# Kernel optimization log

Measured on AMD Instinct MI355X. Metric: run time of the kernel, lower is better.

Reference implementation:

```python
import jax, jax.numpy as jnp
import numpy as np
from jax import lax

HID = 256
CB_N = 512   # codebook_size
CB_D = 64    # codebook_dim
FC = 6       # force_channels
COMMIT_W = 0.25


def _conv(x, w, b, stride):
    # x: [B,C,H,W], w: [O,I,3,3], 'same'-style padding=1
    y = lax.conv_general_dilated(x, w, (stride, stride), ((1, 1), (1, 1)),
                                 dimension_numbers=('NCHW', 'OIHW', 'NCHW'))
    return y + b[None, :, None, None]


def _silu(x):
    return x * jax.nn.sigmoid(x)


def setup_inputs() -> dict:
    key = jax.random.key(0)
    ks = jax.random.split(key, 8)
    s = 0.05
    force_field = jax.random.normal(ks[0], (8, FC, 256, 256), dtype=jnp.float32)
    w1 = jax.random.normal(ks[1], (HID, FC, 3, 3), dtype=jnp.float32) * s
    b1 = jnp.zeros((HID,), dtype=jnp.float32)
    w2 = jax.random.normal(ks[2], (HID, HID, 3, 3), dtype=jnp.float32) * s
    b2 = jnp.zeros((HID,), dtype=jnp.float32)
    w3 = jax.random.normal(ks[3], (CB_D, HID, 3, 3), dtype=jnp.float32) * s
    b3 = jnp.zeros((CB_D,), dtype=jnp.float32)
    codebook = jax.random.uniform(ks[4], (CB_N, CB_D), dtype=jnp.float32,
                                  minval=-1.0 / CB_N, maxval=1.0 / CB_N)
    return {"force_field": force_field, "w1": w1, "b1": b1, "w2": w2,
            "b2": b2, "w3": w3, "b3": b3, "codebook": codebook}


def reference(force_field, w1, b1, w2, b2, w3, b3, codebook):
    # Encoder: conv(pad1) -> SiLU -> conv(stride2) -> SiLU -> conv(stride2)
    h = _silu(_conv(force_field, w1, b1, 1))
    h = _silu(_conv(h, w2, b2, 2))
    z = _conv(h, w3, b3, 2)                      # [B, CB_D, h, w]
    B, C, hh, ww = z.shape
    z_flat = jnp.transpose(z, (0, 2, 3, 1)).reshape(-1, C)  # [N, CB_D]
    # pairwise squared distances: ||z||^2 + ||c||^2 - 2 z.c
    dists = (jnp.sum(z_flat * z_flat, axis=1, keepdims=True)
             + jnp.sum(codebook * codebook, axis=1)
             - 2.0 * (z_flat @ codebook.T))      # [N, CB_N]
    indices = jnp.argmin(dists, axis=1)          # [N] int
    z_q = codebook[indices].reshape(B, hh, ww, C).transpose(0, 3, 1, 2)
    commitment_loss = (jnp.mean((lax.stop_gradient(z_q) - z) ** 2)
                       + COMMIT_W * jnp.mean((z_q - lax.stop_gradient(z)) ** 2))
    tokens = indices.reshape(B, hh, ww)
    return tokens, commitment_loss
```

## Files before the change

### kernel.cpp

```cpp
#include <hip/hip_runtime.h>
#include <math.h>


#define FC    6
#define HID   256
#define CB_N  512
#define CB_D  64

typedef _Float16 f16x8 __attribute__((ext_vector_type(8)));
typedef _Float16 f16x4 __attribute__((ext_vector_type(4)));
typedef float f32x16 __attribute__((ext_vector_type(16)));

#define H1N_IMG    17105920
#define H2N_IMG    4359168

#define FFP_ROW    260
#define FFP_CI     (258 * FFP_ROW)
#define FFP_IMG    (6 * FFP_CI)

__global__ void fill_sentinel_kernel(float* out, int n) {
    int i = blockIdx.x * 256 + threadIdx.x;
    if (i < n) out[i] = -12345.0f;
}

__global__ void h1n_guard_kernel(unsigned int* h1n, int nslots) {
    int i = blockIdx.x * 256 + threadIdx.x;
    if (i >= nslots * 132096) return;
    int slot = i / 132096;
    int r    = i - slot * 132096;
    unsigned int* base = h1n + (size_t)slot * H1N_IMG;
    if (r < 66560) base[r] = 0u;
    else {
        int r2  = r - 66560;
        int j   = r2 & 3;
        int hl  = (r2 >> 2) & 1;
        int cg  = (r2 >> 3) & 31;
        int row = (r2 >> 8) + 1;
        base[(size_t)row * 66560 + 33280 + cg * 1040 + hl * 520 + j] = 0u;
    }
}

__global__ void h2n_guard_kernel(unsigned int* h2n, int nslots) {
    int i = blockIdx.x * 256 + threadIdx.x;
    if (i >= nslots * 66560) return;
    int slot = i / 66560;
    int r    = i - slot * 66560;
    unsigned int* base = h2n + (size_t)slot * H2N_IMG;
    if (r < 33792) base[r] = 0u;
    else {
        int r2  = r - 33792;
        int j   = r2 & 3;
        int hl  = (r2 >> 2) & 1;
        int cg  = (r2 >> 3) & 31;
        int row = (r2 >> 8) + 1;
        base[(size_t)row * 33792 + 16896 + cg * 528 + hl * 264 + j] = 0u;
    }
}

__global__ void wswz1_kernel(const float* __restrict__ w1, _Float16* __restrict__ wsz) {
    int i = blockIdx.x * 256 + threadIdx.x;
    if (i >= 2 * 4 * 4096) return;
    int j   = i & 7;
    int co_ = (i >> 3) & 127;
    int kc  = (i >> 10) & 1;
    int hf  = (i >> 11) & 1;
    int st  = (i >> 12) & 3;
    int ct  = i >> 14;
    int k   = st * 16 + kc * 8 + j;
    int co  = ct * 128 + co_;
    float v = (k < 54) ? w1[(size_t)co * 54 + k] : 0.f;
    _Float16 h = (_Float16)v;
    _Float16 l = (_Float16)(v - (float)h);
    wsz[i] = hf ? l : h;
}

__global__ void wswz2_kernel(const float* __restrict__ w2, _Float16* __restrict__ wsz) {
    int i = blockIdx.x * 256 + threadIdx.x;
    if (i >= 2 * 144 * 4096) return;
    int j   = i & 7;
    int co_ = (i >> 3) & 127;
    int kc  = (i >> 10) & 1;
    int hf  = (i >> 11) & 1;
    int st  = (i >> 12) % 144;
    int ct  = (i >> 12) / 144;
    int ci  = (st & 15) * 16 + kc * 8 + j;
    int rs  = st >> 4;
    float v = w2[(size_t)(ct * 128 + co_) * 2304 + ci * 9 + rs];
    _Float16 h = (_Float16)v;
    _Float16 l = (_Float16)(v - (float)h);
    wsz[i] = hf ? l : h;
}

__global__ void wswz3_kernel(const float* __restrict__ w3, _Float16* __restrict__ wsz) {
    int i = blockIdx.x * 256 + threadIdx.x;
    if (i >= 144 * 2048) return;
    int j  = i & 7;
    int co = (i >> 3) & 63;
    int kc = (i >> 9) & 1;
    int hf = (i >> 10) & 1;
    int st = i >> 11;
    int ci = (st & 15) * 16 + kc * 8 + j;
    int rs = st >> 4;
    float v = w3[(size_t)co * 2304 + ci * 9 + rs];
    _Float16 h = (_Float16)v;
    _Float16 l = (_Float16)(v - (float)h);
    wsz[i] = hf ? l : h;
}

__global__ void cnorm_kernel(const float* __restrict__ cb, float* __restrict__ cn) {
    int j = blockIdx.x * 256 + threadIdx.x;
    if (j < CB_N) {
        const float* p = cb + j * CB_D;
        float s0 = 0.f, s1 = 0.f, s2 = 0.f, s3 = 0.f;
        for (int i = 0; i < CB_D; i += 4) {
            s0 = fmaf(p[i],   p[i],   s0);
            s1 = fmaf(p[i+1], p[i+1], s1);
            s2 = fmaf(p[i+2], p[i+2], s2);
            s3 = fmaf(p[i+3], p[i+3], s3);
        }
        cn[j] = (s0 + s1) + (s2 + s3);
    }
}

__device__ __forceinline__ float silu_f(float v) {
    return v / (1.f + expf(-v));
}

__device__ __forceinline__ unsigned int pack_hl(float v) {
    _Float16 h = (_Float16)v;
    _Float16 l = (_Float16)(v - (float)h);
    unsigned short hb = __builtin_bit_cast(unsigned short, h);
    unsigned short lb = __builtin_bit_cast(unsigned short, l);
    return (unsigned int)hb | ((unsigned int)lb << 16);
}

__device__ __forceinline__ f16x8 as_f16x8(uint4 v) {
    return __builtin_bit_cast(f16x8, v);
}

__device__ __forceinline__ unsigned int ldu32_sb(const char* base, unsigned off, int px) {
    return *(const unsigned int*)(base + (unsigned)__builtin_amdgcn_readfirstlane((int)off) + px * 4);
}

__device__ __forceinline__ void sync_lds() {
    asm volatile("s_waitcnt lgkmcnt(0)\n\ts_barrier" ::: "memory");
}

__global__ __launch_bounds__(256) void ffpack_kernel(const float* __restrict__ ff,
                                                     unsigned int* __restrict__ ffp) {
    const int gw   = (blockIdx.x * 256 + threadIdx.x) >> 6;
    const int lane = threadIdx.x & 63;
    const int y  = gw & 255;
    const int ic = gw >> 8;
    const float* rowp = ff + ((size_t)ic * 256 + y) * 256;
    float4 v = *(const float4*)(rowp + 4 * lane);
    unsigned p0 = pack_hl(v.x), p1 = pack_hl(v.y), p2 = pack_hl(v.z), p3 = pack_hl(v.w);
    unsigned p3p = __shfl_up(p3, 1);
    if (lane == 0) p3p = 0u;
    unsigned int* orow = ffp + ((size_t)ic * 258 + y + 1) * FFP_ROW;
    uint4 o; o.x = p3p; o.y = p0; o.z = p1; o.w = p2;
    *(uint4*)(orow + 4 * lane) = o;
    if (lane == 63) { orow[256] = p3; orow[257] = 0u; }
}

__global__ __launch_bounds__(256) void conv1_mfma_kernel(
        const unsigned int* __restrict__ ffp,
        const _Float16* __restrict__ wsz1,
        const float* __restrict__ bias,
        unsigned int* __restrict__ h1n,
        int b0) {
    __shared__ __align__(16) _Float16 ldsA[2][2][128][8];
    __shared__ __align__(16) _Float16 ldsB[2][128][24];
    __shared__ __align__(16) unsigned int T[64];
    __shared__ float biasl[128];

    const int tid = threadIdx.x;
    const int py  = blockIdx.x >> 1;
    const int xt  = blockIdx.x & 1;
    const int ct  = blockIdx.y;
    const int img = blockIdx.z;

    const unsigned int* ffpi = ffp + (size_t)(b0 + img) * FFP_IMG;
    _Float16* h1f = (_Float16*)(h1n + (size_t)img * H1N_IMG);

    if (tid < 64) {
        int k = tid;
        unsigned off;
        if (k < 54) {
            int ci  = k / 9;
            int tap = k - ci * 9;
            int r   = tap / 3;
            int s   = tap - r * 3;
            off = (unsigned)((((size_t)ci * 258 + py + r) * FFP_ROW + xt * 128 + s) * 4);
        } else {
            off = (unsigned)((xt * 128) * 4);
        }
        T[k] = off;
    }
    if (tid < 128) biasl[tid] = bias[ct * 128 + tid];
    __syncthreads();

    const int lane = tid & 63;
    const int w    = tid >> 6;
    const int cow  = (w >> 1) * 64;
    const int pxw  = (w & 1) * 64;
    const int m_   = lane & 31;
    const int kc   = lane >> 5;
    const int px   = tid & 127;
    const int kh   = tid >> 7;

    f32x16 acc[2][2];
    #pragma unroll
    for (int a = 0; a < 2; a++)
        #pragma unroll
        for (int b = 0; b < 2; b++)
            #pragma unroll
            for (int r = 0; r < 16; r++) acc[a][b][r] = 0.f;

    uint4* aldsf = (uint4*)&ldsA[0][0][0][0];
    const char* gbase = (const char*)ffpi;

    uint4 a0, a1;
    unsigned v0, v1, v2, v3, v4, v5, v6, v7;
    {
        const uint4* ag = (const uint4*)(wsz1 + ((size_t)(ct * 4)) * 4096);
        a0 = ag[tid];
        a1 = ag[tid + 256];
        const int k0 = kh * 8;
        uint4 rb0 = *(const uint4*)&T[k0];
        uint4 rb1 = *(const uint4*)&T[k0 + 4];
        v0 = ldu32_sb(gbase, rb0.x, px); v1 = ldu32_sb(gbase, rb0.y, px);
        v2 = ldu32_sb(gbase, rb0.z, px); v3 = ldu32_sb(gbase, rb0.w, px);
        v4 = ldu32_sb(gbase, rb1.x, px); v5 = ldu32_sb(gbase, rb1.y, px);
        v6 = ldu32_sb(gbase, rb1.z, px); v7 = ldu32_sb(gbase, rb1.w, px);
    }

    for (int t = 0; t < 4; t++) {
        sync_lds();

        aldsf[tid]       = a0;
        aldsf[tid + 256] = a1;
        uint4 bh, bl;
        bh.x = (v0 & 0xffffu) | (v1 << 16);
        bh.y = (v2 & 0xffffu) | (v3 << 16);
        bh.z = (v4 & 0xffffu) | (v5 << 16);
        bh.w = (v6 & 0xffffu) | (v7 << 16);
        bl.x = (v0 >> 16) | (v1 & 0xffff0000u);
        bl.y = (v2 >> 16) | (v3 & 0xffff0000u);
        bl.z = (v4 >> 16) | (v5 & 0xffff0000u);
        bl.w = (v6 >> 16) | (v7 & 0xffff0000u);
        *(uint4*)&ldsB[0][px][kh * 8] = bh;
        *(uint4*)&ldsB[1][px][kh * 8] = bl;

        sync_lds();

        if (t < 3) {
            const uint4* ag = (const uint4*)(wsz1 + ((size_t)(ct * 4 + t + 1)) * 4096);
            a0 = ag[tid];
            a1 = ag[tid + 256];
            const int k0 = (t + 1) * 16 + kh * 8;
            uint4 rb0 = *(const uint4*)&T[k0 & 63];
            uint4 rb1 = *(const uint4*)&T[(k0 + 4) & 63];
            v0 = ldu32_sb(gbase, rb0.x, px); v1 = ldu32_sb(gbase, rb0.y, px);
            v2 = ldu32_sb(gbase, rb0.z, px); v3 = ldu32_sb(gbase, rb0.w, px);
            v4 = ldu32_sb(gbase, rb1.x, px); v5 = ldu32_sb(gbase, rb1.y, px);
            v6 = ldu32_sb(gbase, rb1.z, px); v7 = ldu32_sb(gbase, rb1.w, px);
        }

        f16x8 ah0 = *(const f16x8*)&ldsA[0][kc][cow + m_][0];
        f16x8 ah1 = *(const f16x8*)&ldsA[0][kc][cow + 32 + m_][0];
        f16x8 al0 = *(const f16x8*)&ldsA[1][kc][cow + m_][0];
        f16x8 al1 = *(const f16x8*)&ldsA[1][kc][cow + 32 + m_][0];
        f16x8 xh0 = *(const f16x8*)&ldsB[0][pxw + m_][kc * 8];
        f16x8 xh1 = *(const f16x8*)&ldsB[0][pxw + 32 + m_][kc * 8];
        f16x8 xl0 = *(const f16x8*)&ldsB[1][pxw + m_][kc * 8];
        f16x8 xl1 = *(const f16x8*)&ldsB[1][pxw + 32 + m_][kc * 8];

        acc[0][0] = __builtin_amdgcn_mfma_f32_32x32x16_f16(ah0, xh0, acc[0][0], 0, 0, 0);
        acc[0][1] = __builtin_amdgcn_mfma_f32_32x32x16_f16(ah0, xh1, acc[0][1], 0, 0, 0);
        acc[1][0] = __builtin_amdgcn_mfma_f32_32x32x16_f16(ah1, xh0, acc[1][0], 0, 0, 0);
        acc[1][1] = __builtin_amdgcn_mfma_f32_32x32x16_f16(ah1, xh1, acc[1][1], 0, 0, 0);
        acc[0][0] = __builtin_amdgcn_mfma_f32_32x32x16_f16(ah0, xl0, acc[0][0], 0, 0, 0);
        acc[0][1] = __builtin_amdgcn_mfma_f32_32x32x16_f16(ah0, xl1, acc[0][1], 0, 0, 0);
        acc[1][0] = __builtin_amdgcn_mfma_f32_32x32x16_f16(ah1, xl0, acc[1][0], 0, 0, 0);
        acc[1][1] = __builtin_amdgcn_mfma_f32_32x32x16_f16(ah1, xl1, acc[1][1], 0, 0, 0);
        acc[0][0] = __builtin_amdgcn_mfma_f32_32x32x16_f16(al0, xh0, acc[0][0], 0, 0, 0);
        acc[0][1] = __builtin_amdgcn_mfma_f32_32x32x16_f16(al0, xh1, acc[0][1], 0, 0, 0);
        acc[1][0] = __builtin_amdgcn_mfma_f32_32x32x16_f16(al1, xh0, acc[1][0], 0, 0, 0);
        acc[1][1] = __builtin_amdgcn_mfma_f32_32x32x16_f16(al1, xh1, acc[1][1], 0, 0, 0);
    }

    #pragma unroll
    for (int mt = 0; mt < 2; mt++) {
        #pragma unroll
        for (int nt = 0; nt < 2; nt++) {
            const int pxo = xt * 128 + pxw + nt * 32 + m_;
            const int par = pxo & 1;
            const int xs  = par ? ((pxo + 1) >> 1) : (pxo >> 1);
            _Float16* dst = h1f + (size_t)(py + 1) * 133120 + par * 66560 + xs * 8 + kc * 4;
            #pragma unroll
            for (int q = 0; q < 4; q++) {
                const int cb_ = cow + mt * 32 + 8 * q + 4 * kc;
                const int cg  = (ct * 128 + cow + mt * 32 + 8 * q) >> 3;
                f16x4 oh, ol;
                #pragma unroll
                for (int j = 0; j < 4; j++) {
                    float v = silu_f(acc[mt][nt][4*q+j] + biasl[cb_ + j]);
                    _Float16 h = (_Float16)v;
                    oh[j] = h;
                    ol[j] = (_Float16)(v - (float)h);
                }
                *(f16x4*)(dst + (size_t)cg * 2080)        = oh;
                *(f16x4*)(dst + (size_t)cg * 2080 + 1040) = ol;
            }
        }
    }
}

__global__ __launch_bounds__(256) void conv2_mfma_kernel(
        const unsigned int* __restrict__ h1n,
        const _Float16* __restrict__ wsz2,
        const float* __restrict__ bias,
        unsigned int* __restrict__ h2n) {
    __shared__ __align__(16) char ldsB[2 * 16384];
    __shared__ float biasl[128];

    const int tid = threadIdx.x;
    const int py  = blockIdx.x;
    const int ct  = blockIdx.y;
    const int img = blockIdx.z;

    if (tid < 128) biasl[tid] = bias[ct * 128 + tid];

    const int lane = tid & 63;
    const int w    = tid >> 6;
    const int cow  = (w >> 1) * 64;
    const int pxw  = (w & 1) * 64;
    const int m_   = lane & 31;
    const int kc   = lane >> 5;

    const char* bbase = (const char*)(h1n + (size_t)img * H1N_IMG);
    const char* abase = (const char*)wsz2 + (size_t)ct * 144 * 8192
                        + (size_t)kc * 2048 + (size_t)(cow + m_) * 16;

    const int spx = tid & 127;
    const int skc = tid >> 7;
    const unsigned sgfix = (unsigned)(skc * 4160 + spx * 16);
    const unsigned swfix = (unsigned)(skc * 2048 + spx * 16);
    const unsigned rfix0 = (unsigned)(kc * 2048 + (pxw + m_) * 16);
    const unsigned rfix1 = (unsigned)(kc * 2048 + (pxw + 32 + m_) * 16);

    auto offu = [&](int t) -> unsigned {
        int rs = t >> 4;
        int r  = (rs * 11) >> 5;
        int s  = rs - 3 * r;
        return (unsigned)((2 * py + r) * 266240 + (s != 1 ? 133120 : 0)
                          + (s == 2 ? 16 : 0) + (t & 15) * 8320);
    };

    f32x16 acc[2][2];
    #pragma unroll
    for (int a = 0; a < 2; a++)
        #pragma unroll
        for (int b = 0; b < 2; b++)
            #pragma unroll
            for (int r = 0; r < 16; r++) acc[a][b][r] = 0.f;

    uint4 pa0, pa1, pa2, pa3;
    uint4 wa0, wa1, wa2, wa3;
    uint4 wb0, wb1, wb2, wb3;
    {
        pa0 = *(const uint4*)(abase);
        pa1 = *(const uint4*)(abase + 512);
        pa2 = *(const uint4*)(abase + 4096);
        pa3 = *(const uint4*)(abase + 4096 + 512);
        unsigned o0 = offu(0);
        uint4 th = *(const uint4*)(bbase + o0 + sgfix);
        uint4 tl = *(const uint4*)(bbase + o0 + sgfix + 2080);
        *(uint4*)(ldsB + swfix)        = th;
        *(uint4*)(ldsB + 4096 + swfix) = tl;
        unsigned o1 = offu(1);
        th = *(const uint4*)(bbase + o1 + sgfix);
        tl = *(const uint4*)(bbase + o1 + sgfix + 2080);
        *(uint4*)(ldsB + 8192 + swfix)  = th;
        *(uint4*)(ldsB + 12288 + swfix) = tl;
        unsigned o2 = offu(2);
        wa0 = *(const uint4*)(bbase + o2 + sgfix);
        wa1 = *(const uint4*)(bbase + o2 + sgfix + 2080);
        unsigned o3 = offu(3);
        wa2 = *(const uint4*)(bbase + o3 + sgfix);
        wa3 = *(const uint4*)(bbase + o3 + sgfix + 2080);
        unsigned o4 = offu(4);
        wb0 = *(const uint4*)(bbase + o4 + sgfix);
        wb1 = *(const uint4*)(bbase + o4 + sgfix + 2080);
        unsigned o5 = offu(5);
        wb2 = *(const uint4*)(bbase + o5 + sgfix);
        wb3 = *(const uint4*)(bbase + o5 + sgfix + 2080);
    }
    sync_lds();

    auto superstep = [&](int s, uint4& W0, uint4& W1, uint4& W2, uint4& W3) {
        const int t0 = 2 * s;
        char* rslot = ldsB + (s & 1) * 16384;

        if (s < 71) {
            char* wslot = ldsB + ((s + 1) & 1) * 16384;
            *(uint4*)(wslot + swfix)         = W0;
            *(uint4*)(wslot + 4096 + swfix)  = W1;
            *(uint4*)(wslot + 8192 + swfix)  = W2;
            *(uint4*)(wslot + 12288 + swfix) = W3;
        }
        if (s < 69) {
            unsigned oa = offu(t0 + 6);
            unsigned ob = offu(t0 + 7);
            W0 = *(const uint4*)(bbase + oa + sgfix);
            W1 = *(const uint4*)(bbase + oa + sgfix + 2080);
            W2 = *(const uint4*)(bbase + ob + sgfix);
            W3 = *(const uint4*)(bbase + ob + sgfix + 2080);
        }

        f16x8 xh0 = *(const f16x8*)(rslot + rfix0);
        f16x8 xl0 = *(const f16x8*)(rslot + 4096 + rfix0);
        f16x8 xh1 = *(const f16x8*)(rslot + rfix1);
        f16x8 xl1 = *(const f16x8*)(rslot + 4096 + rfix1);

        uint4 ca0 = pa0, ca1 = pa1, ca2 = pa2, ca3 = pa3;
        {
            const char* ap = abase + (size_t)(t0 + 1) * 8192;
            pa0 = *(const uint4*)(ap);
            pa1 = *(const uint4*)(ap + 512);
            pa2 = *(const uint4*)(ap + 4096);
            pa3 = *(const uint4*)(ap + 4096 + 512);
        }

        f16x8 ah0 = as_f16x8(ca0);
        f16x8 ah1 = as_f16x8(ca1);
        f16x8 al0 = as_f16x8(ca2);
        f16x8 al1 = as_f16x8(ca3);

        acc[0][0] = __builtin_amdgcn_mfma_f32_32x32x16_f16(ah0, xh0, acc[0][0], 0, 0, 0);
        acc[0][1] = __builtin_amdgcn_mfma_f32_32x32x16_f16(ah0, xh1, acc[0][1], 0, 0, 0);
        acc[1][0] = __builtin_amdgcn_mfma_f32_32x32x16_f16(ah1, xh0, acc[1][0], 0, 0, 0);
        acc[1][1] = __builtin_amdgcn_mfma_f32_32x32x16_f16(ah1, xh1, acc[1][1], 0, 0, 0);
        acc[0][0] = __builtin_amdgcn_mfma_f32_32x32x16_f16(ah0, xl0, acc[0][0], 0, 0, 0);
        acc[0][1] = __builtin_amdgcn_mfma_f32_32x32x16_f16(ah0, xl1, acc[0][1], 0, 0, 0);
        acc[1][0] = __builtin_amdgcn_mfma_f32_32x32x16_f16(ah1, xl0, acc[1][0], 0, 0, 0);
        acc[1][1] = __builtin_amdgcn_mfma_f32_32x32x16_f16(ah1, xl1, acc[1][1], 0, 0, 0);
        acc[0][0] = __builtin_amdgcn_mfma_f32_32x32x16_f16(al0, xh0, acc[0][0], 0, 0, 0);
        acc[0][1] = __builtin_amdgcn_mfma_f32_32x32x16_f16(al0, xh1, acc[0][1], 0, 0, 0);
        acc[1][0] = __builtin_amdgcn_mfma_f32_32x32x16_f16(al1, xh0, acc[1][0], 0, 0, 0);
        acc[1][1] = __builtin_amdgcn_mfma_f32_32x32x16_f16(al1, xh1, acc[1][1], 0, 0, 0);

        f16x8 yh0 = *(const f16x8*)(rslot + 8192 + rfix0);
        f16x8 yl0 = *(const f16x8*)(rslot + 12288 + rfix0);
        f16x8 yh1 = *(const f16x8*)(rslot + 8192 + rfix1);
        f16x8 yl1 = *(const f16x8*)(rslot + 12288 + rfix1);

        ca0 = pa0; ca1 = pa1; ca2 = pa2; ca3 = pa3;
        if (s < 71) {
            const char* ap = abase + (size_t)(t0 + 2) * 8192;
            pa0 = *(const uint4*)(ap);
            pa1 = *(const uint4*)(ap + 512);
            pa2 = *(const uint4*)(ap + 4096);
            pa3 = *(const uint4*)(ap + 4096 + 512);
        }

        ah0 = as_f16x8(ca0);
        ah1 = as_f16x8(ca1);
        al0 = as_f16x8(ca2);
        al1 = as_f16x8(ca3);

        acc[0][0] = __builtin_amdgcn_mfma_f32_32x32x16_f16(ah0, yh0, acc[0][0], 0, 0, 0);
        acc[0][1] = __builtin_amdgcn_mfma_f32_32x32x16_f16(ah0, yh1, acc[0][1], 0, 0, 0);
        acc[1][0] = __builtin_amdgcn_mfma_f32_32x32x16_f16(ah1, yh0, acc[1][0], 0, 0, 0);
        acc[1][1] = __builtin_amdgcn_mfma_f32_32x32x16_f16(ah1, yh1, acc[1][1], 0, 0, 0);
        acc[0][0] = __builtin_amdgcn_mfma_f32_32x32x16_f16(ah0, yl0, acc[0][0], 0, 0, 0);
        acc[0][1] = __builtin_amdgcn_mfma_f32_32x32x16_f16(ah0, yl1, acc[0][1], 0, 0, 0);
        acc[1][0] = __builtin_amdgcn_mfma_f32_32x32x16_f16(ah1, yl0, acc[1][0], 0, 0, 0);
        acc[1][1] = __builtin_amdgcn_mfma_f32_32x32x16_f16(ah1, yl1, acc[1][1], 0, 0, 0);
        acc[0][0] = __builtin_amdgcn_mfma_f32_32x32x16_f16(al0, yh0, acc[0][0], 0, 0, 0);
        acc[0][1] = __builtin_amdgcn_mfma_f32_32x32x16_f16(al0, yh1, acc[0][1], 0, 0, 0);
        acc[1][0] = __builtin_amdgcn_mfma_f32_32x32x16_f16(al1, yh0, acc[1][0], 0, 0, 0);
        acc[1][1] = __builtin_amdgcn_mfma_f32_32x32x16_f16(al1, yh1, acc[1][1], 0, 0, 0);

        sync_lds();
    };

    for (int ss = 0; ss < 36; ss++) {
        superstep(2 * ss,     wa0, wa1, wa2, wa3);
        superstep(2 * ss + 1, wb0, wb1, wb2, wb3);
    }

    _Float16* h2f = (_Float16*)(h2n + (size_t)img * H2N_IMG);
    #pragma unroll
    for (int mt = 0; mt < 2; mt++) {
        #pragma unroll
        for (int nt = 0; nt < 2; nt++) {
            const int pxo = pxw + nt * 32 + m_;
            const int par = pxo & 1;
            const int xs  = par ? ((pxo + 1) >> 1) : (pxo >> 1);
            _Float16* dst = h2f + (size_t)(py + 1) * 67584 + par * 33792 + xs * 8 + kc * 4;
            #pragma unroll
            for (int q = 0; q < 4; q++) {
                const int cb_ = cow + mt * 32 + 8 * q + 4 * kc;
                const int cg  = (ct * 128 + cow + mt * 32 + 8 * q) >> 3;
                f16x4 oh, ol;
                #pragma unroll
                for (int j = 0; j < 4; j++) {
                    float v = silu_f(acc[mt][nt][4*q+j] + biasl[cb_ + j]);
                    _Float16 h = (_Float16)v;
                    oh[j] = h;
                    ol[j] = (_Float16)(v - (float)h);
                }
                *(f16x4*)(dst + (size_t)cg * 1056)       = oh;
                *(f16x4*)(dst + (size_t)cg * 1056 + 528) = ol;
            }
        }
    }
}

__global__ __launch_bounds__(64) void conv3_mfma_kernel(
        const unsigned int* __restrict__ h2n,
        const _Float16* __restrict__ wsz3,
        const float* __restrict__ bias,
        float* __restrict__ z) {
    const int bi  = blockIdx.x;
    const int img = blockIdx.y;
    const int py  = bi >> 2;
    const int ct3 = (bi >> 1) & 1;
    const int pxt = bi & 1;

    const int lane = threadIdx.x;
    const int m_   = lane & 31;
    const int kc   = lane >> 5;

    const char* bbase = (const char*)(h2n + (size_t)img * H2N_IMG);
    const char* abase = (const char*)wsz3 + (size_t)kc * 1024 + (size_t)(ct3 * 32 + m_) * 16;
    const unsigned bfix = (unsigned)(kc * 2112 + (pxt * 32 + m_) * 16);

    auto offu = [&](int t) -> unsigned {
        int rs = t >> 4;
        int r  = (rs * 11) >> 5;
        int s  = rs - 3 * r;
        return (unsigned)((2 * py + r) * 135168 + (s != 1 ? 67584 : 0)
                          + (s == 2 ? 16 : 0) + (t & 15) * 4224);
    };

    f32x16 acc;
    #pragma unroll
    for (int r = 0; r < 16; r++) acc[r] = 0.f;

    uint4 rh[8], rl[8];
    #pragma unroll
    for (int i = 0; i < 8; i++) {
        unsigned o = offu(i);
        rh[i] = *(const uint4*)(bbase + o + bfix);
        rl[i] = *(const uint4*)(bbase + o + bfix + 1056);
    }
    uint4 pa0 = *(const uint4*)(abase);
    uint4 pa1 = *(const uint4*)(abase + 2048);

    for (int tb = 0; tb < 144; tb += 8) {
        #pragma unroll
        for (int i = 0; i < 8; i++) {
            const int t = tb + i;
            uint4 cbh = rh[i], cbl = rl[i];
            if (t + 8 < 144) {
                unsigned o = offu(t + 8);
                rh[i] = *(const uint4*)(bbase + o + bfix);
                rl[i] = *(const uint4*)(bbase + o + bfix + 1056);
            }
            uint4 ca0 = pa0, ca1 = pa1;
            if (t < 143) {
                const char* ap = abase + (size_t)(t + 1) * 4096;
                pa0 = *(const uint4*)(ap);
                pa1 = *(const uint4*)(ap + 2048);
            }
            f16x8 ah = as_f16x8(ca0);
            f16x8 al = as_f16x8(ca1);
            f16x8 xh = as_f16x8(cbh);
            f16x8 xl = as_f16x8(cbl);
            acc = __builtin_amdgcn_mfma_f32_32x32x16_f16(ah, xh, acc, 0, 0, 0);
            acc = __builtin_amdgcn_mfma_f32_32x32x16_f16(ah, xl, acc, 0, 0, 0);
            acc = __builtin_amdgcn_mfma_f32_32x32x16_f16(al, xh, acc, 0, 0, 0);
        }
    }

    const int x = pxt * 32 + m_;
    float* zp = z + (((size_t)img * 64 + py) * 64 + x) * 64;
    #pragma unroll
    for (int q = 0; q < 4; q++) {
        const int co = ct3 * 32 + 8 * q + 4 * kc;
        float4 o;
        o.x = acc[4*q+0] + bias[co + 0];
        o.y = acc[4*q+1] + bias[co + 1];
        o.z = acc[4*q+2] + bias[co + 2];
        o.w = acc[4*q+3] + bias[co + 3];
        *(float4*)(zp + co) = o;
    }
}

__global__ __launch_bounds__(128) void vqpart_kernel(const float* __restrict__ z,
                                                     const float* __restrict__ cb,
                                                     const float* __restrict__ cn,
                                                     float* __restrict__ part_d,
                                                     int* __restrict__ part_i) {
    __shared__ __align__(16) float lds_cb[128 * 64];
    __shared__ float lds_cn[128];

    const int tid = threadIdx.x;
    const int q   = blockIdx.y;
    const int n   = blockIdx.x * 128 + tid;

    #pragma unroll
    for (int i = 0; i < 16; i++) {
        const int f4 = tid + 128 * i;
        *(float4*)&lds_cb[f4 * 4] = *(const float4*)(cb + q * 8192 + f4 * 4);
    }
    lds_cn[tid] = cn[q * 128 + tid];
    __syncthreads();

    float zr[64];
    const float* zp = z + (size_t)n * 64;
    #pragma unroll
    for (int i = 0; i < 16; i++)
        *(float4*)&zr[i * 4] = *(const float4*)(zp + i * 4);

    float zn0 = 0.f, zn1 = 0.f, zn2 = 0.f, zn3 = 0.f;
    #pragma unroll
    for (int i = 0; i < 64; i += 4) {
        zn0 = fmaf(zr[i],   zr[i],   zn0);
        zn1 = fmaf(zr[i+1], zr[i+1], zn1);
        zn2 = fmaf(zr[i+2], zr[i+2], zn2);
        zn3 = fmaf(zr[i+3], zr[i+3], zn3);
    }
    const float znorm = (zn0 + zn1) + (zn2 + zn3);

    float dmin = 1e30f;
    int best = 0;
    for (int j = 0; j < 128; j++) {
        const float* cp = &lds_cb[j * 64];
        float d0 = 0.f, d1 = 0.f, d2 = 0.f, d3 = 0.f;
        #pragma unroll
        for (int i = 0; i < 16; i++) {
            const float4 c4 = *(const float4*)&cp[i * 4];
            d0 = fmaf(zr[i*4],   c4.x, d0);
            d1 = fmaf(zr[i*4+1], c4.y, d1);
            d2 = fmaf(zr[i*4+2], c4.z, d2);
            d3 = fmaf(zr[i*4+3], c4.w, d3);
        }
        const float dot = (d0 + d1) + (d2 + d3);
        const float d = (znorm + lds_cn[j]) - 2.f * dot;
        if (d < dmin) { dmin = d; best = q * 128 + j; }
    }

    part_d[(size_t)q * 32768 + n] = dmin;
    part_i[(size_t)q * 32768 + n] = best;
}

__global__ __launch_bounds__(256) void vqred_kernel(const float* __restrict__ z,
                                                    const float* __restrict__ cb,
                                                    const float* __restrict__ part_d,
                                                    const int* __restrict__ part_i,
                                                    float* __restrict__ tokens_out,
                                                    float* __restrict__ loss_accum) {
    __shared__ float red[4];
    const int tid = threadIdx.x;
    const int n   = blockIdx.x * 256 + tid;

    float dmin = part_d[n];
    int   best = part_i[n];
    #pragma unroll
    for (int q = 1; q < 4; q++) {
        float d = part_d[(size_t)q * 32768 + n];
        int   i = part_i[(size_t)q * 32768 + n];
        if (d < dmin) { dmin = d; best = i; }
    }
    tokens_out[n] = (float)best;

    float zr[64];
    const float* zp = z + (size_t)n * 64;
    #pragma unroll
    for (int i = 0; i < 16; i++)
        *(float4*)&zr[i * 4] = *(const float4*)(zp + i * 4);

    const float* cbest = cb + (size_t)best * 64;
    float l0 = 0.f, l1 = 0.f, l2 = 0.f, l3 = 0.f;
    #pragma unroll
    for (int i = 0; i < 64; i += 4) {
        float t0 = cbest[i]     - zr[i];
        float t1 = cbest[i + 1] - zr[i + 1];
        float t2 = cbest[i + 2] - zr[i + 2];
        float t3 = cbest[i + 3] - zr[i + 3];
        l0 = fmaf(t0, t0, l0);
        l1 = fmaf(t1, t1, l1);
        l2 = fmaf(t2, t2, l2);
        l3 = fmaf(t3, t3, l3);
    }
    float l = (l0 + l1) + (l2 + l3);
    #pragma unroll
    for (int off = 32; off > 0; off >>= 1)
        l += __shfl_down(l, off);
    if ((tid & 63) == 0) red[tid >> 6] = l;
    __syncthreads();
    if (tid == 0)
        atomicAdd(loss_accum, (red[0] + red[1]) + (red[2] + red[3]));
}

__global__ void finalize_kernel(const float* __restrict__ loss_accum,
                                float* __restrict__ out_loss) {
    const float m = loss_accum[0] / 2097152.f;
    out_loss[0] = m + 0.25f * m;
}

extern "C" void kernel_launch(void* const* d_in, const int* in_sizes, int n_in,
                              void* d_out, int out_size, void* d_ws, size_t ws_size,
                              hipStream_t stream) {
    const float* ff = (const float*)d_in[0];
    const float* w1 = (const float*)d_in[1];
    const float* b1 = (const float*)d_in[2];
    const float* w2 = (const float*)d_in[3];
    const float* b2 = (const float*)d_in[4];
    const float* w3 = (const float*)d_in[5];
    const float* b3 = (const float*)d_in[6];
    const float* cb = (const float*)d_in[7];
    float* out = (float*)d_out;
    float* ws  = (float*)d_ws;

    const size_t TAIL = 2097152 + 8 * (size_t)FFP_IMG + 589824 + 147456 + 16384
                      + 512 + 131072 + 131072 + 1;
    auto need_u32 = [&](int nimg) -> size_t {
        return (size_t)nimg * (H1N_IMG + H2N_IMG) + TAIL;
    };

    int nimg;
    if      (ws_size >= need_u32(8) * 4) nimg = 8;
    else if (ws_size >= need_u32(4) * 4) nimg = 4;
    else if (ws_size >= need_u32(2) * 4) nimg = 2;
    else {
        fill_sentinel_kernel<<<(out_size + 255) / 256, 256, 0, stream>>>(out, out_size);
        return;
    }

    unsigned int* h1n  = (unsigned int*)ws;
    unsigned int* h2n  = h1n + (size_t)nimg * H1N_IMG;
    float*        zbuf = (float*)(h2n + (size_t)nimg * H2N_IMG);
    unsigned int* ffp  = (unsigned int*)(zbuf + 2097152);
    _Float16* wsz2 = (_Float16*)(ffp + 8 * (size_t)FFP_IMG);
    _Float16* wsz3 = wsz2 + 1179648;
    _Float16* wsz1 = wsz3 + 294912;
    float*    cn   = (float*)(wsz1 + 32768);
    float*    pd   = cn + 512;
    int*      pi   = (int*)(pd + 131072);
    float*    lacc = (float*)(pi + 131072);

    hipMemsetAsync(ffp, 0, 8 * (size_t)FFP_IMG * 4, stream);
    h1n_guard_kernel<<<(nimg * 132096 + 255) / 256, 256, 0, stream>>>(h1n, nimg);
    h2n_guard_kernel<<<(nimg * 66560 + 255) / 256, 256, 0, stream>>>(h2n, nimg);
    wswz1_kernel<<<(2 * 4 * 4096 + 255) / 256, 256, 0, stream>>>(w1, wsz1);
    wswz2_kernel<<<(2 * 144 * 4096 + 255) / 256, 256, 0, stream>>>(w2, wsz2);
    wswz3_kernel<<<(144 * 2048 + 255) / 256, 256, 0, stream>>>(w3, wsz3);
    cnorm_kernel<<<2, 256, 0, stream>>>(cb, cn);
    ffpack_kernel<<<3072, 256, 0, stream>>>(ff, ffp);

    for (int b0 = 0; b0 < 8; b0 += nimg) {
        conv1_mfma_kernel<<<dim3(512, 2, nimg), 256, 0, stream>>>(ffp, wsz1, b1, h1n, b0);
        conv2_mfma_kernel<<<dim3(128, 2, nimg), 256, 0, stream>>>(h1n, wsz2, b2, h2n);
        conv3_mfma_kernel<<<dim3(256, nimg), 64, 0, stream>>>(
            h2n, wsz3, b3, zbuf + (size_t)b0 * 262144);
    }

    hipMemsetAsync(lacc, 0, sizeof(float), stream);
    vqpart_kernel<<<dim3(256, 4), 128, 0, stream>>>(zbuf, cb, cn, pd, pi);
    vqred_kernel<<<128, 256, 0, stream>>>(zbuf, cb, pd, pi, out, lacc);
    finalize_kernel<<<1, 1, 0, stream>>>(lacc, out + 32768);
}
```

Before: 940.0 us.

## Split conv2 reduction across two wave groups with LDS partial-sum combine

Conv2 blocks grow from 256 to 512 threads. Each half of the block processes half of the 144 K-steps (72 each) in its own double-buffered LDS region, and the two partial accumulators are then summed through LDS before the SiLU/split-f16 epilogue. The aim is more waves per output tile and more latency hiding, since the original grid of 128x2xnimg blocks gives limited parallelism. In exchange it doubles LDS per block, adds a block-wide sync and LDS round-trip for the reduction, and leaves half the threads idle during the epilogue.

```diff
diff --git a/kernel.cpp b/kernel.cpp
--- a/kernel.cpp
+++ b/kernel.cpp
@@ -317,23 +317,22 @@
     }
 }
 
-__global__ __launch_bounds__(256) void conv2_mfma_kernel(
+__global__ __launch_bounds__(512, 4) void conv2_mfma_kernel(
         const unsigned int* __restrict__ h1n,
         const _Float16* __restrict__ wsz2,
         const float* __restrict__ bias,
         unsigned int* __restrict__ h2n) {
-    __shared__ __align__(16) char ldsB[2 * 16384];
-    __shared__ float biasl[128];
-
-    const int tid = threadIdx.x;
+    __shared__ __align__(16) char ldsB[4 * 16384];
+
+    const int tid  = threadIdx.x;
+    const int kz   = tid >> 8;
+    const int ltid = tid & 255;
     const int py  = blockIdx.x;
     const int ct  = blockIdx.y;
     const int img = blockIdx.z;
 
-    if (tid < 128) biasl[tid] = bias[ct * 128 + tid];
-
     const int lane = tid & 63;
-    const int w    = tid >> 6;
+    const int w    = (tid >> 6) & 3;
     const int cow  = (w >> 1) * 64;
     const int pxw  = (w & 1) * 64;
     const int m_   = lane & 31;
@@ -341,16 +340,20 @@
 
     const char* bbase = (const char*)(h1n + (size_t)img * H1N_IMG);
     const char* abase = (const char*)wsz2 + (size_t)ct * 144 * 8192
+                        + (size_t)kz * 72 * 8192
                         + (size_t)kc * 2048 + (size_t)(cow + m_) * 16;
-
-    const int spx = tid & 127;
-    const int skc = tid >> 7;
+    char* myB = ldsB + kz * 32768;
+
+    const int spx = ltid & 127;
+    const int skc = ltid >> 7;
     const unsigned sgfix = (unsigned)(skc * 4160 + spx * 16);
     const unsigned swfix = (unsigned)(skc * 2048 + spx * 16);
     const unsigned rfix0 = (unsigned)(kc * 2048 + (pxw + m_) * 16);
     const unsigned rfix1 = (unsigned)(kc * 2048 + (pxw + 32 + m_) * 16);
 
+    const int tofs = kz * 72;
     auto offu = [&](int t) -> unsigned {
+        t += tofs;
         int rs = t >> 4;
         int r  = (rs * 11) >> 5;
         int s  = rs - 3 * r;
@@ -377,13 +380,13 @@
         unsigned o0 = offu(0);
         uint4 th = *(const uint4*)(bbase + o0 + sgfix);
         uint4 tl = *(const uint4*)(bbase + o0 + sgfix + 2080);
-        *(uint4*)(ldsB + swfix)        = th;
-        *(uint4*)(ldsB + 4096 + swfix) = tl;
+        *(uint4*)(myB + swfix)        = th;
+        *(uint4*)(myB + 4096 + swfix) = tl;
         unsigned o1 = offu(1);
         th = *(const uint4*)(bbase + o1 + sgfix);
         tl = *(const uint4*)(bbase + o1 + sgfix + 2080);
-        *(uint4*)(ldsB + 8192 + swfix)  = th;
-        *(uint4*)(ldsB + 12288 + swfix) = tl;
+        *(uint4*)(myB + 8192 + swfix)  = th;
+        *(uint4*)(myB + 12288 + swfix) = tl;
         unsigned o2 = offu(2);
         wa0 = *(const uint4*)(bbase + o2 + sgfix);
         wa1 = *(const uint4*)(bbase + o2 + sgfix + 2080);
@@ -401,16 +404,16 @@
 
     auto superstep = [&](int s, uint4& W0, uint4& W1, uint4& W2, uint4& W3) {
         const int t0 = 2 * s;
-        char* rslot = ldsB + (s & 1) * 16384;
-
-        if (s < 71) {
-            char* wslot = ldsB + ((s + 1) & 1) * 16384;
+        char* rslot = myB + (s & 1) * 16384;
+
+        if (s < 35) {
+            char* wslot = myB + ((s + 1) & 1) * 16384;
             *(uint4*)(wslot + swfix)         = W0;
             *(uint4*)(wslot + 4096 + swfix)  = W1;
             *(uint4*)(wslot + 8192 + swfix)  = W2;
             *(uint4*)(wslot + 12288 + swfix) = W3;
         }
-        if (s < 69) {
+        if (s < 33) {
             unsigned oa = offu(t0 + 6);
             unsigned ob = offu(t0 + 7);
             W0 = *(const uint4*)(bbase + oa + sgfix);
@@ -457,7 +460,7 @@
         f16x8 yl1 = *(const f16x8*)(rslot + 12288 + rfix1);
 
         ca0 = pa0; ca1 = pa1; ca2 = pa2; ca3 = pa3;
-        if (s < 71) {
+        if (s < 35) {
             const char* ap = abase + (size_t)(t0 + 2) * 8192;
             pa0 = *(const uint4*)(ap);
             pa1 = *(const uint4*)(ap + 512);
@@ -486,34 +489,68 @@
         sync_lds();
     };
 
-    for (int ss = 0; ss < 36; ss++) {
+    for (int ss = 0; ss < 18; ss++) {
         superstep(2 * ss,     wa0, wa1, wa2, wa3);
         superstep(2 * ss + 1, wb0, wb1, wb2, wb3);
     }
 
-    _Float16* h2f = (_Float16*)(h2n + (size_t)img * H2N_IMG);
-    #pragma unroll
-    for (int mt = 0; mt < 2; mt++) {
+    if (kz) {
         #pragma unroll
-        for (int nt = 0; nt < 2; nt++) {
-            const int pxo = pxw + nt * 32 + m_;
-            const int par = pxo & 1;
-            const int xs  = par ? ((pxo + 1) >> 1) : (pxo >> 1);
-            _Float16* dst = h2f + (size_t)(py + 1) * 67584 + par * 33792 + xs * 8 + kc * 4;
+        for (int a = 0; a < 2; a++)
             #pragma unroll
-            for (int q = 0; q < 4; q++) {
-                const int cb_ = cow + mt * 32 + 8 * q + 4 * kc;
-                const int cg  = (ct * 128 + cow + mt * 32 + 8 * q) >> 3;
-                f16x4 oh, ol;
+            for (int b = 0; b < 2; b++)
                 #pragma unroll
-                for (int j = 0; j < 4; j++) {
-                    float v = silu_f(acc[mt][nt][4*q+j] + biasl[cb_ + j]);
-                    _Float16 h = (_Float16)v;
-                    oh[j] = h;
-                    ol[j] = (_Float16)(v - (float)h);
+                for (int r = 0; r < 4; r++) {
+                    const int c = (a * 2 + b) * 4 + r;
+                    float4 v;
+                    v.x = acc[a][b][4*r+0];
+                    v.y = acc[a][b][4*r+1];
+                    v.z = acc[a][b][4*r+2];
+                    v.w = acc[a][b][4*r+3];
+                    *(float4*)(ldsB + ((size_t)c * 256 + ltid) * 16) = v;
                 }
-                *(f16x4*)(dst + (size_t)cg * 1056)       = oh;
-                *(f16x4*)(dst + (size_t)cg * 1056 + 528) = ol;
+    }
+    __syncthreads();
+    if (kz == 0) {
+        #pragma unroll
+        for (int a = 0; a < 2; a++)
+            #pragma unroll
+            for (int b = 0; b < 2; b++)
+                #pragma unroll
+                for (int r = 0; r < 4; r++) {
+                    const int c = (a * 2 + b) * 4 + r;
+                    const float4 v = *(const float4*)(ldsB + ((size_t)c * 256 + ltid) * 16);
+                    acc[a][b][4*r+0] += v.x;
+                    acc[a][b][4*r+1] += v.y;
+                    acc[a][b][4*r+2] += v.z;
+                    acc[a][b][4*r+3] += v.w;
+                }
+
+        const float* bp = bias + ct * 128;
+        _Float16* h2f = (_Float16*)(h2n + (size_t)img * H2N_IMG);
+        #pragma unroll
+        for (int mt = 0; mt < 2; mt++) {
+            #pragma unroll
+            for (int nt = 0; nt < 2; nt++) {
+                const int pxo = pxw + nt * 32 + m_;
+                const int par = pxo & 1;
+                const int xs  = par ? ((pxo + 1) >> 1) : (pxo >> 1);
+                _Float16* dst = h2f + (size_t)(py + 1) * 67584 + par * 33792 + xs * 8 + kc * 4;
+                #pragma unroll
+                for (int q = 0; q < 4; q++) {
+                    const int cb_ = cow + mt * 32 + 8 * q + 4 * kc;
+                    const int cg  = (ct * 128 + cow + mt * 32 + 8 * q) >> 3;
+                    f16x4 oh, ol;
+                    #pragma unroll
+                    for (int j = 0; j < 4; j++) {
+                        float v = silu_f(acc[mt][nt][4*q+j] + bp[cb_ + j]);
+                        _Float16 h = (_Float16)v;
+                        oh[j] = h;
+                        ol[j] = (_Float16)(v - (float)h);
+                    }
+                    *(f16x4*)(dst + (size_t)cg * 1056)       = oh;
+                    *(f16x4*)(dst + (size_t)cg * 1056 + 528) = ol;
+                }
             }
         }
     }
@@ -765,7 +802,7 @@
 
     for (int b0 = 0; b0 < 8; b0 += nimg) {
         conv1_mfma_kernel<<<dim3(512, 2, nimg), 256, 0, stream>>>(ffp, wsz1, b1, h1n, b0);
-        conv2_mfma_kernel<<<dim3(128, 2, nimg), 256, 0, stream>>>(h1n, wsz2, b2, h2n);
+        conv2_mfma_kernel<<<dim3(128, 2, nimg), 512, 0, stream>>>(h1n, wsz2, b2, h2n);
         conv3_mfma_kernel<<<dim3(256, nimg), 64, 0, stream>>>(
             h2n, wsz3, b3, zbuf + (size_t)b0 * 262144);
     }
```

Measured after the change: 1.077 ms. +14.6%, slower.

## Split conv2 pixel tile in half to double grid and raise occupancy

Applied to the files above, without the earlier changes.

Each conv2 block now covers 64 output pixels instead of 128, so the grid doubles along x. Each wave holds two accumulators instead of four, the LDS staging buffer is halved and per-thread prefetch registers drop, with launch bounds asking for four blocks per CU. The aim is more resident waves to hide global and LDS latency. In exchange, every weight tile is loaded by twice as many blocks, which halves weight reuse per block and raises weight traffic.

```diff
diff --git a/kernel.cpp b/kernel.cpp
--- a/kernel.cpp
+++ b/kernel.cpp
@@ -317,16 +317,17 @@
     }
 }
 
-__global__ __launch_bounds__(256) void conv2_mfma_kernel(
+__global__ __launch_bounds__(256, 4) void conv2_mfma_kernel(
         const unsigned int* __restrict__ h1n,
         const _Float16* __restrict__ wsz2,
         const float* __restrict__ bias,
         unsigned int* __restrict__ h2n) {
-    __shared__ __align__(16) char ldsB[2 * 16384];
+    __shared__ __align__(16) char ldsB[2 * 8192];
     __shared__ float biasl[128];
 
     const int tid = threadIdx.x;
-    const int py  = blockIdx.x;
+    const int py  = blockIdx.x >> 1;
+    const int xt  = blockIdx.x & 1;
     const int ct  = blockIdx.y;
     const int img = blockIdx.z;
 
@@ -335,7 +336,7 @@
     const int lane = tid & 63;
     const int w    = tid >> 6;
     const int cow  = (w >> 1) * 64;
-    const int pxw  = (w & 1) * 64;
+    const int pxw  = (w & 1) * 32;
     const int m_   = lane & 31;
     const int kc   = lane >> 5;
 
@@ -343,12 +344,12 @@
     const char* abase = (const char*)wsz2 + (size_t)ct * 144 * 8192
                         + (size_t)kc * 2048 + (size_t)(cow + m_) * 16;
 
-    const int spx = tid & 127;
-    const int skc = tid >> 7;
-    const unsigned sgfix = (unsigned)(skc * 4160 + spx * 16);
-    const unsigned swfix = (unsigned)(skc * 2048 + spx * 16);
-    const unsigned rfix0 = (unsigned)(kc * 2048 + (pxw + m_) * 16);
-    const unsigned rfix1 = (unsigned)(kc * 2048 + (pxw + 32 + m_) * 16);
+    const int spx = tid & 63;
+    const int skc = (tid >> 6) & 1;
+    const int shl = tid >> 7;
+    const unsigned sgfix = (unsigned)(skc * 4160 + spx * 16 + xt * 1024 + shl * 2080);
+    const unsigned swfix = (unsigned)(shl * 2048 + skc * 1024 + spx * 16);
+    const unsigned rfix0 = (unsigned)(kc * 1024 + (pxw + m_) * 16);
 
     auto offu = [&](int t) -> unsigned {
         int rs = t >> 4;
@@ -358,71 +359,47 @@
                           + (s == 2 ? 16 : 0) + (t & 15) * 8320);
     };
 
-    f32x16 acc[2][2];
+    f32x16 acc[2];
     #pragma unroll
     for (int a = 0; a < 2; a++)
         #pragma unroll
-        for (int b = 0; b < 2; b++)
-            #pragma unroll
-            for (int r = 0; r < 16; r++) acc[a][b][r] = 0.f;
+        for (int r = 0; r < 16; r++) acc[a][r] = 0.f;
 
     uint4 pa0, pa1, pa2, pa3;
-    uint4 wa0, wa1, wa2, wa3;
-    uint4 wb0, wb1, wb2, wb3;
+    uint4 wa0, wa1;
+    uint4 wb0, wb1;
     {
         pa0 = *(const uint4*)(abase);
         pa1 = *(const uint4*)(abase + 512);
         pa2 = *(const uint4*)(abase + 4096);
         pa3 = *(const uint4*)(abase + 4096 + 512);
-        unsigned o0 = offu(0);
-        uint4 th = *(const uint4*)(bbase + o0 + sgfix);
-        uint4 tl = *(const uint4*)(bbase + o0 + sgfix + 2080);
-        *(uint4*)(ldsB + swfix)        = th;
-        *(uint4*)(ldsB + 4096 + swfix) = tl;
-        unsigned o1 = offu(1);
-        th = *(const uint4*)(bbase + o1 + sgfix);
-        tl = *(const uint4*)(bbase + o1 + sgfix + 2080);
-        *(uint4*)(ldsB + 8192 + swfix)  = th;
-        *(uint4*)(ldsB + 12288 + swfix) = tl;
-        unsigned o2 = offu(2);
-        wa0 = *(const uint4*)(bbase + o2 + sgfix);
-        wa1 = *(const uint4*)(bbase + o2 + sgfix + 2080);
-        unsigned o3 = offu(3);
-        wa2 = *(const uint4*)(bbase + o3 + sgfix);
-        wa3 = *(const uint4*)(bbase + o3 + sgfix + 2080);
-        unsigned o4 = offu(4);
-        wb0 = *(const uint4*)(bbase + o4 + sgfix);
-        wb1 = *(const uint4*)(bbase + o4 + sgfix + 2080);
-        unsigned o5 = offu(5);
-        wb2 = *(const uint4*)(bbase + o5 + sgfix);
-        wb3 = *(const uint4*)(bbase + o5 + sgfix + 2080);
+        uint4 t0v = *(const uint4*)(bbase + offu(0) + sgfix);
+        *(uint4*)(ldsB + swfix) = t0v;
+        uint4 t1v = *(const uint4*)(bbase + offu(1) + sgfix);
+        *(uint4*)(ldsB + 4096 + swfix) = t1v;
+        wa0 = *(const uint4*)(bbase + offu(2) + sgfix);
+        wa1 = *(const uint4*)(bbase + offu(3) + sgfix);
+        wb0 = *(const uint4*)(bbase + offu(4) + sgfix);
+        wb1 = *(const uint4*)(bbase + offu(5) + sgfix);
     }
     sync_lds();
 
-    auto superstep = [&](int s, uint4& W0, uint4& W1, uint4& W2, uint4& W3) {
+    auto superstep = [&](int s, uint4& W0, uint4& W1) {
         const int t0 = 2 * s;
-        char* rslot = ldsB + (s & 1) * 16384;
+        char* rslot = ldsB + (s & 1) * 8192;
 
         if (s < 71) {
-            char* wslot = ldsB + ((s + 1) & 1) * 16384;
-            *(uint4*)(wslot + swfix)         = W0;
-            *(uint4*)(wslot + 4096 + swfix)  = W1;
-            *(uint4*)(wslot + 8192 + swfix)  = W2;
-            *(uint4*)(wslot + 12288 + swfix) = W3;
+            char* wslot = ldsB + ((s + 1) & 1) * 8192;
+            *(uint4*)(wslot + swfix)        = W0;
+            *(uint4*)(wslot + 4096 + swfix) = W1;
         }
         if (s < 69) {
-            unsigned oa = offu(t0 + 6);
-            unsigned ob = offu(t0 + 7);
-            W0 = *(const uint4*)(bbase + oa + sgfix);
-            W1 = *(const uint4*)(bbase + oa + sgfix + 2080);
-            W2 = *(const uint4*)(bbase + ob + sgfix);
-            W3 = *(const uint4*)(bbase + ob + sgfix + 2080);
+            W0 = *(const uint4*)(bbase + offu(t0 + 6) + sgfix);
+            W1 = *(const uint4*)(bbase + offu(t0 + 7) + sgfix);
         }
 
         f16x8 xh0 = *(const f16x8*)(rslot + rfix0);
-        f16x8 xl0 = *(const f16x8*)(rslot + 4096 + rfix0);
-        f16x8 xh1 = *(const f16x8*)(rslot + rfix1);
-        f16x8 xl1 = *(const f16x8*)(rslot + 4096 + rfix1);
+        f16x8 xl0 = *(const f16x8*)(rslot + 2048 + rfix0);
 
         uint4 ca0 = pa0, ca1 = pa1, ca2 = pa2, ca3 = pa3;
         {
@@ -438,23 +415,15 @@
         f16x8 al0 = as_f16x8(ca2);
         f16x8 al1 = as_f16x8(ca3);
 
-        acc[0][0] = __builtin_amdgcn_mfma_f32_32x32x16_f16(ah0, xh0, acc[0][0], 0, 0, 0);
-        acc[0][1] = __builtin_amdgcn_mfma_f32_32x32x16_f16(ah0, xh1, acc[0][1], 0, 0, 0);
-        acc[1][0] = __builtin_amdgcn_mfma_f32_32x32x16_f16(ah1, xh0, acc[1][0], 0, 0, 0);
-        acc[1][1] = __builtin_amdgcn_mfma_f32_32x32x16_f16(ah1, xh1, acc[1][1], 0, 0, 0);
-        acc[0][0] = __builtin_amdgcn_mfma_f32_32x32x16_f16(ah0, xl0, acc[0][0], 0, 0, 0);
-        acc[0][1] = __builtin_amdgcn_mfma_f32_32x32x16_f16(ah0, xl1, acc[0][1], 0, 0, 0);
-        acc[1][0] = __builtin_amdgcn_mfma_f32_32x32x16_f16(ah1, xl0, acc[1][0], 0, 0, 0);
-        acc[1][1] = __builtin_amdgcn_mfma_f32_32x32x16_f16(ah1, xl1, acc[1][1], 0, 0, 0);
-        acc[0][0] = __builtin_amdgcn_mfma_f32_32x32x16_f16(al0, xh0, acc[0][0], 0, 0, 0);
-        acc[0][1] = __builtin_amdgcn_mfma_f32_32x32x16_f16(al0, xh1, acc[0][1], 0, 0, 0);
-        acc[1][0] = __builtin_amdgcn_mfma_f32_32x32x16_f16(al1, xh0, acc[1][0], 0, 0, 0);
-        acc[1][1] = __builtin_amdgcn_mfma_f32_32x32x16_f16(al1, xh1, acc[1][1], 0, 0, 0);
-
-        f16x8 yh0 = *(const f16x8*)(rslot + 8192 + rfix0);
-        f16x8 yl0 = *(const f16x8*)(rslot + 12288 + rfix0);
-        f16x8 yh1 = *(const f16x8*)(rslot + 8192 + rfix1);
-        f16x8 yl1 = *(const f16x8*)(rslot + 12288 + rfix1);
+        acc[0] = __builtin_amdgcn_mfma_f32_32x32x16_f16(ah0, xh0, acc[0], 0, 0, 0);
+        acc[1] = __builtin_amdgcn_mfma_f32_32x32x16_f16(ah1, xh0, acc[1], 0, 0, 0);
+        acc[0] = __builtin_amdgcn_mfma_f32_32x32x16_f16(ah0, xl0, acc[0], 0, 0, 0);
+        acc[1] = __builtin_amdgcn_mfma_f32_32x32x16_f16(ah1, xl0, acc[1], 0, 0, 0);
+        acc[0] = __builtin_amdgcn_mfma_f32_32x32x16_f16(al0, xh0, acc[0], 0, 0, 0);
+        acc[1] = __builtin_amdgcn_mfma_f32_32x32x16_f16(al1, xh0, acc[1], 0, 0, 0);
+
+        f16x8 yh0 = *(const f16x8*)(rslot + 4096 + rfix0);
+        f16x8 yl0 = *(const f16x8*)(rslot + 6144 + rfix0);
 
         ca0 = pa0; ca1 = pa1; ca2 = pa2; ca3 = pa3;
         if (s < 71) {
@@ -470,51 +439,42 @@
         al0 = as_f16x8(ca2);
         al1 = as_f16x8(ca3);
 
-        acc[0][0] = __builtin_amdgcn_mfma_f32_32x32x16_f16(ah0, yh0, acc[0][0], 0, 0, 0);
-        acc[0][1] = __builtin_amdgcn_mfma_f32_32x32x16_f16(ah0, yh1, acc[0][1], 0, 0, 0);
-        acc[1][0] = __builtin_amdgcn_mfma_f32_32x32x16_f16(ah1, yh0, acc[1][0], 0, 0, 0);
-        acc[1][1] = __builtin_amdgcn_mfma_f32_32x32x16_f16(ah1, yh1, acc[1][1], 0, 0, 0);
-        acc[0][0] = __builtin_amdgcn_mfma_f32_32x32x16_f16(ah0, yl0, acc[0][0], 0, 0, 0);
-        acc[0][1] = __builtin_amdgcn_mfma_f32_32x32x16_f16(ah0, yl1, acc[0][1], 0, 0, 0);
-        acc[1][0] = __builtin_amdgcn_mfma_f32_32x32x16_f16(ah1, yl0, acc[1][0], 0, 0, 0);
-        acc[1][1] = __builtin_amdgcn_mfma_f32_32x32x16_f16(ah1, yl1, acc[1][1], 0, 0, 0);
-        acc[0][0] = __builtin_amdgcn_mfma_f32_32x32x16_f16(al0, yh0, acc[0][0], 0, 0, 0);
-        acc[0][1] = __builtin_amdgcn_mfma_f32_32x32x16_f16(al0, yh1, acc[0][1], 0, 0, 0);
-        acc[1][0] = __builtin_amdgcn_mfma_f32_32x32x16_f16(al1, yh0, acc[1][0], 0, 0, 0);
-        acc[1][1] = __builtin_amdgcn_mfma_f32_32x32x16_f16(al1, yh1, acc[1][1], 0, 0, 0);
+        acc[0] = __builtin_amdgcn_mfma_f32_32x32x16_f16(ah0, yh0, acc[0], 0, 0, 0);
+        acc[1] = __builtin_amdgcn_mfma_f32_32x32x16_f16(ah1, yh0, acc[1], 0, 0, 0);
+        acc[0] = __builtin_amdgcn_mfma_f32_32x32x16_f16(ah0, yl0, acc[0], 0, 0, 0);
+        acc[1] = __builtin_amdgcn_mfma_f32_32x32x16_f16(ah1, yl0, acc[1], 0, 0, 0);
+        acc[0] = __builtin_amdgcn_mfma_f32_32x32x16_f16(al0, yh0, acc[0], 0, 0, 0);
+        acc[1] = __builtin_amdgcn_mfma_f32_32x32x16_f16(al1, yh0, acc[1], 0, 0, 0);
 
         sync_lds();
     };
 
     for (int ss = 0; ss < 36; ss++) {
-        superstep(2 * ss,     wa0, wa1, wa2, wa3);
-        superstep(2 * ss + 1, wb0, wb1, wb2, wb3);
+        superstep(2 * ss,     wa0, wa1);
+        superstep(2 * ss + 1, wb0, wb1);
     }
 
     _Float16* h2f = (_Float16*)(h2n + (size_t)img * H2N_IMG);
+    const int pxo = xt * 64 + pxw + m_;
+    const int par = pxo & 1;
+    const int xs  = par ? ((pxo + 1) >> 1) : (pxo >> 1);
+    _Float16* dst = h2f + (size_t)(py + 1) * 67584 + par * 33792 + xs * 8 + kc * 4;
     #pragma unroll
     for (int mt = 0; mt < 2; mt++) {
         #pragma unroll
-        for (int nt = 0; nt < 2; nt++) {
-            const int pxo = pxw + nt * 32 + m_;
-            const int par = pxo & 1;
-            const int xs  = par ? ((pxo + 1) >> 1) : (pxo >> 1);
-            _Float16* dst = h2f + (size_t)(py + 1) * 67584 + par * 33792 + xs * 8 + kc * 4;
+        for (int q = 0; q < 4; q++) {
+            const int cb_ = cow + mt * 32 + 8 * q + 4 * kc;
+            const int cg  = (ct * 128 + cow + mt * 32 + 8 * q) >> 3;
+            f16x4 oh, ol;
             #pragma unroll
-            for (int q = 0; q < 4; q++) {
-                const int cb_ = cow + mt * 32 + 8 * q + 4 * kc;
-                const int cg  = (ct * 128 + cow + mt * 32 + 8 * q) >> 3;
-                f16x4 oh, ol;
-                #pragma unroll
-                for (int j = 0; j < 4; j++) {
-                    float v = silu_f(acc[mt][nt][4*q+j] + biasl[cb_ + j]);
-                    _Float16 h = (_Float16)v;
-                    oh[j] = h;
-                    ol[j] = (_Float16)(v - (float)h);
-                }
-                *(f16x4*)(dst + (size_t)cg * 1056)       = oh;
-                *(f16x4*)(dst + (size_t)cg * 1056 + 528) = ol;
+            for (int j = 0; j < 4; j++) {
+                float v = silu_f(acc[mt][4*q+j] + biasl[cb_ + j]);
+                _Float16 h = (_Float16)v;
+                oh[j] = h;
+                ol[j] = (_Float16)(v - (float)h);
             }
+            *(f16x4*)(dst + (size_t)cg * 1056)       = oh;
+            *(f16x4*)(dst + (size_t)cg * 1056 + 528) = ol;
         }
     }
 }
@@ -765,7 +725,7 @@
 
     for (int b0 = 0; b0 < 8; b0 += nimg) {
         conv1_mfma_kernel<<<dim3(512, 2, nimg), 256, 0, stream>>>(ffp, wsz1, b1, h1n, b0);
-        conv2_mfma_kernel<<<dim3(128, 2, nimg), 256, 0, stream>>>(h1n, wsz2, b2, h2n);
+        conv2_mfma_kernel<<<dim3(256, 2, nimg), 256, 0, stream>>>(h1n, wsz2, b2, h2n);
         conv3_mfma_kernel<<<dim3(256, nimg), 64, 0, stream>>>(
             h2n, wsz3, b3, zbuf + (size_t)b0 * 262144);
     }
```

Measured after the change: 912.7 us. -2.9%, faster.
